# Kernel tuning notes

Measured on AMD Instinct MI355X. Metric: run time of the kernel, lower is better.

The kernel has to match this reference:

```python
import jax, jax.numpy as jnp
import numpy as np

B, T, TR, D, H = 8, 1024, 256, 1024, 16
HS = D // H  # head size = 64
FF = 4 * D


def _ln(x, g, b, eps=1e-5):
    m = jnp.mean(x, axis=-1, keepdims=True)
    v = jnp.mean((x - m) ** 2, axis=-1, keepdims=True)
    return (x - m) * jax.lax.rsqrt(v + eps) * g + b


def setup_inputs() -> dict:
    key = jax.random.key(0)
    ks = jax.random.split(key, 24)
    w = lambda i, shape: jax.random.normal(ks[i], shape, dtype=jnp.float32) * 0.02
    return {
        "x": jax.random.normal(ks[0], (B, T, D), dtype=jnp.float32),
        # reduced positional embedding table (gathered by arange == table itself)
        "pos_emb": w(1, (TR, D)),
        # inner standard Block params
        "blk_ln1_g": jnp.ones((D,), jnp.float32), "blk_ln1_b": jnp.zeros((D,), jnp.float32),
        "blk_wq": w(2, (H, D, HS)), "blk_wk": w(3, (H, D, HS)), "blk_wv": w(4, (H, D, HS)),
        "blk_wo": w(5, (D, D)), "blk_bo": jnp.zeros((D,), jnp.float32),
        "blk_ln2_g": jnp.ones((D,), jnp.float32), "blk_ln2_b": jnp.zeros((D,), jnp.float32),
        "blk_w1": w(6, (D, FF)), "blk_b1": jnp.zeros((FF,), jnp.float32),
        "blk_w2": w(7, (FF, D)), "blk_b2": jnp.zeros((D,), jnp.float32),
        # compressing cross-attention params
        "ln1_g": jnp.ones((D,), jnp.float32), "ln1_b": jnp.zeros((D,), jnp.float32),
        "ca_wq": w(8, (H, D, HS)), "ca_wk": w(9, (H, D, HS)), "ca_wv": w(10, (H, D, HS)),
        "ca_wo": w(11, (D, D)), "ca_bo": jnp.zeros((D,), jnp.float32),
        "ln2_g": jnp.ones((D,), jnp.float32), "ln2_b": jnp.zeros((D,), jnp.float32),
        "ff_w1": w(12, (D, FF)), "ff_b1": jnp.zeros((FF,), jnp.float32),
        "ff_w2": w(13, (FF, D)), "ff_b2": jnp.zeros((D,), jnp.float32),
    }


def reference(x, pos_emb, blk_ln1_g, blk_ln1_b, blk_wq, blk_wk, blk_wv, blk_wo, blk_bo,
              blk_ln2_g, blk_ln2_b, blk_w1, blk_b1, blk_w2, blk_b2,
              ln1_g, ln1_b, ca_wq, ca_wk, ca_wv, ca_wo, ca_bo,
              ln2_g, ln2_b, ff_w1, ff_b1, ff_w2, ff_b2):
    b, t, c = x.shape
    scale = c ** -0.5  # matches q @ k^T * c**-0.5 in source

    # ---- inner standard Block: y = x + sa(ln1(x)); y = y + ffwd(ln2(y)) ----
    h = _ln(x, blk_ln1_g, blk_ln1_b)
    q = jnp.einsum('btc,hcs->bhts', h, blk_wq)
    k = jnp.einsum('btc,hcs->bhts', h, blk_wk)
    v = jnp.einsum('btc,hcs->bhts', h, blk_wv)
    wei = jnp.einsum('bhts,bhus->bhtu', q, k) * scale
    causal = jnp.tril(jnp.ones((t, t), dtype=bool))
    wei = jax.nn.softmax(jnp.where(causal, wei, -jnp.inf), axis=-1)
    att = jnp.einsum('bhtu,bhus->bhts', wei, v)
    att = att.transpose(0, 2, 1, 3).reshape(b, t, c) @ blk_wo + blk_bo
    y = x + att
    h2 = _ln(y, blk_ln2_g, blk_ln2_b)
    y = y + (jax.nn.relu(h2 @ blk_w1 + blk_b1) @ blk_w2 + blk_b2)

    # outer residual in CompressingBlock.forward
    x = x + y

    # ---- compressing cross-attention: queries/values from x, keys from pos emb ----
    h1 = _ln(x, ln1_g, ln1_b)
    q = jnp.einsum('btc,hcs->bhts', h1, ca_wq)
    kk = jnp.einsum('rc,hcs->hrs', pos_emb, ca_wk)  # same for every batch
    v = jnp.einsum('btc,hcs->bhts', h1, ca_wv)
    wei = jnp.einsum('bhts,hrs->bhtr', q, kk) * scale  # [b,h,t,tr]
    tr = pos_emb.shape[0]
    mask = jnp.tril(jnp.ones((t, tr), dtype=bool))  # tril[:t,:tr]
    wei = jax.nn.softmax(jnp.where(mask, wei, -jnp.inf), axis=-1)
    # transpose then wei^T @ v -> compressed sequence length tr
    out = jnp.einsum('bhtr,bhts->bhrs', wei, v)
    out = out.transpose(0, 2, 1, 3).reshape(b, tr, c) @ ca_wo + ca_bo

    # ---- final FFN with residual ----
    h3 = _ln(out, ln2_g, ln2_b)
    out = out + (jax.nn.relu(h3 @ ff_w1 + ff_b1) @ ff_w2 + ff_b2)
    return out
```

## Files before the change

kernel.cpp:

```cpp
#include <hip/hip_runtime.h>
#include <stdint.h>

typedef unsigned short u16;
typedef __attribute__((ext_vector_type(8))) short short8;
typedef __attribute__((ext_vector_type(4))) float f32x4;

#define MFMA16(A,B,C) __builtin_amdgcn_mfma_f32_16x16x32_bf16(A,B,C,0,0,0)

static __device__ __forceinline__ u16 f2bf(float f) {
  union { float f; unsigned u; } v; v.f = f;
  unsigned r = v.u + 0x7FFFu + ((v.u >> 16) & 1u);
  return (u16)(r >> 16);
}

static __device__ __forceinline__ void gload16(const void* g, void* l) {
  __builtin_amdgcn_global_load_lds(
      (const __attribute__((address_space(1))) void*)(uintptr_t)g,
      (__attribute__((address_space(3))) void*)(uint32_t)(uintptr_t)l,
      16, 0, 0);
}

static __device__ __forceinline__ int xcd_swz() {
  const int gx = gridDim.x, gy = gridDim.y, nwg = gx * gy;
  const int orig = blockIdx.y * gx + blockIdx.x;
  const int q = nwg >> 3, rm = nwg & 7, xcd = orig & 7, idx = orig >> 3;
  return (xcd < rm ? xcd * (q + 1) : rm * (q + 1) + (xcd - rm) * q) + idx;
}

#define GPH(CUR, STAGE_STMT, TAIL_STMT) do { \
  short8 af_[4], bf_[4]; \
  _Pragma("unroll") \
  for (int mf = 0; mf < 4; ++mf) { \
    const int r = wm0 + mf * 16 + colL; \
    af_[mf] = *(const short8*)&lds[(CUR) + r * 32 + ((kgr ^ ((r >> 1) & 3)) << 3)]; \
  } \
  _Pragma("unroll") \
  for (int nf = 0; nf < 4; ++nf) { \
    const int r = wn0 + nf * 16 + colL; \
    bf_[nf] = *(const short8*)&lds[(CUR) + 4096 + r * 32 + ((kgr ^ ((r >> 1) & 3)) << 3)]; \
  } \
  STAGE_STMT; \
  _Pragma("unroll") \
  for (int mf = 0; mf < 4; ++mf) \
    _Pragma("unroll") \
    for (int nf = 0; nf < 4; ++nf) \
      acc[mf][nf] = MFMA16(af_[mf], bf_[nf], acc[mf][nf]); \
  TAIL_STMT; \
  __builtin_amdgcn_sched_barrier(0); \
  __builtin_amdgcn_s_barrier(); \
  asm volatile("" ::: "memory"); \
} while (0)

__global__ __launch_bounds__(256) void gemm128p(
    const u16* __restrict__ A, const u16* __restrict__ Wt,
    float* __restrict__ Cf, u16* __restrict__ Cb,
    const float* __restrict__ bias,
    const float* __restrict__ res1, const float* __restrict__ res2,
    int M, int N, int K, int relu)
{
  __shared__ u16 lds[24576];
  const int tid = threadIdx.x;
  const int wid = tid >> 6, lane = tid & 63;
  const int colL = lane & 15, kgr = lane >> 4;
  const int wm0 = (wid & 1) * 64, wn0 = (wid >> 1) * 64;
  const int w = xcd_swz();
  const int m0 = (w / gridDim.y) * 128, n0 = (w % gridDim.y) * 128;
  const int U = K >> 5;
  f32x4 acc[4][4] = {};

  auto stageP = [&](int u, int bufo) {
    const int kb = u * 32;
#pragma unroll
    for (int i = 0; i < 2; ++i) {
      const int c = i * 256 + tid;
      const int row = c >> 2, slot = c & 3;
      const int cs = kb + ((slot ^ ((row >> 1) & 3)) << 3);
      gload16(A  + (size_t)(m0 + row) * K + cs,
              &lds[bufo + ((i * 256 + wid * 64) << 3)]);
      gload16(Wt + (size_t)(n0 + row) * K + cs,
              &lds[bufo + 4096 + ((i * 256 + wid * 64) << 3)]);
    }
  };

  int c0 = 0, c1 = 8192, c2 = 16384;
  stageP(0, c0); stageP(1, c1);
  asm volatile("s_waitcnt vmcnt(4)" ::: "memory");
  __builtin_amdgcn_s_barrier();
  asm volatile("" ::: "memory");

  for (int u = 0; u < U; ++u) {
    GPH(c0,
        { if (u + 2 < U) stageP(u + 2, c2); },
        { if (u + 2 < U) { asm volatile("s_waitcnt vmcnt(4)" ::: "memory"); }
          else           { asm volatile("s_waitcnt vmcnt(0)" ::: "memory"); } });
    const int tmp = c0; c0 = c1; c1 = c2; c2 = tmp;
  }

#pragma unroll
  for (int mf = 0; mf < 4; ++mf) {
#pragma unroll
    for (int nf = 0; nf < 4; ++nf) {
      const int n = n0 + wn0 + nf * 16 + colL;
      const float bv = bias ? bias[n] : 0.f;
#pragma unroll
      for (int rr = 0; rr < 4; ++rr) {
        const int m = m0 + wm0 + mf * 16 + kgr * 4 + rr;
        const size_t off = (size_t)m * N + n;
        float v = acc[mf][nf][rr] + bv;
        if (res1) v += res1[off];
        if (res2) v += res2[off];
        if (relu) v = fmaxf(v, 0.f);
        if (Cf) Cf[off] = v; else Cb[off] = f2bf(v);
      }
    }
  }
}

__global__ __launch_bounds__(256) void ln_rows(
    const float* __restrict__ x, const float* __restrict__ g,
    const float* __restrict__ bt, u16* __restrict__ out)
{
  const int row = blockIdx.x, tid = threadIdx.x;
  const float4 v = ((const float4*)(x + (size_t)row * 1024))[tid];
  float s  = v.x + v.y + v.z + v.w;
  float ss = v.x * v.x + v.y * v.y + v.z * v.z + v.w * v.w;
#pragma unroll
  for (int off = 32; off; off >>= 1) {
    s  += __shfl_xor(s, off);
    ss += __shfl_xor(ss, off);
  }
  __shared__ float red[8];
  const int wid = tid >> 6, lane = tid & 63;
  if (lane == 0) { red[wid] = s; red[4 + wid] = ss; }
  __syncthreads();
  s  = red[0] + red[1] + red[2] + red[3];
  ss = red[4] + red[5] + red[6] + red[7];
  const float mean = s * 0.0009765625f;
  const float var  = ss * 0.0009765625f - mean * mean;
  const float rstd = rsqrtf(var + 1e-5f);
  const float4 gg = ((const float4*)g)[tid];
  const float4 bb = ((const float4*)bt)[tid];
  uint2 ov;
  ov.x = (unsigned)f2bf((v.x - mean) * rstd * gg.x + bb.x) |
         ((unsigned)f2bf((v.y - mean) * rstd * gg.y + bb.y) << 16);
  ov.y = (unsigned)f2bf((v.z - mean) * rstd * gg.z + bb.z) |
         ((unsigned)f2bf((v.w - mean) * rstd * gg.w + bb.w) << 16);
  *(uint2*)(out + (size_t)row * 1024 + tid * 4) = ov;
}

__global__ __launch_bounds__(256) void transpose_w(
    const float* __restrict__ in, u16* __restrict__ out, int R, int C)
{
  __shared__ float t[32][33];
  const int c0 = blockIdx.x * 32, r0 = blockIdx.y * 32;
  const int tx = threadIdx.x & 31, ty = threadIdx.x >> 5;
#pragma unroll
  for (int i = 0; i < 32; i += 8)
    t[ty + i][tx] = in[(size_t)(r0 + ty + i) * C + c0 + tx];
  __syncthreads();
#pragma unroll
  for (int i = 0; i < 32; i += 8)
    out[(size_t)(c0 + ty + i) * R + r0 + tx] = f2bf(t[tx][ty + i]);
}

__global__ __launch_bounds__(256) void pack_head_w(
    const float* __restrict__ w, u16* __restrict__ out)
{
  __shared__ float t[32][33];
  const int h = blockIdx.z;
  const int s0 = blockIdx.x * 32, c0 = blockIdx.y * 32;
  const int tx = threadIdx.x & 31, ty = threadIdx.x >> 5;
#pragma unroll
  for (int i = 0; i < 32; i += 8)
    t[ty + i][tx] = w[((size_t)h * 1024 + c0 + ty + i) * 64 + s0 + tx];
  __syncthreads();
#pragma unroll
  for (int i = 0; i < 32; i += 8)
    out[((size_t)h * 64 + s0 + ty + i) * 1024 + c0 + tx] = f2bf(t[tx][ty + i]);
}

__global__ __launch_bounds__(256) void cvt_bf16(
    const float* __restrict__ in, u16* __restrict__ out)
{
  const int i = blockIdx.x * blockDim.x + threadIdx.x;
  const float4 v = ((const float4*)in)[i];
  uint2 ov;
  ov.x = (unsigned)f2bf(v.x) | ((unsigned)f2bf(v.y) << 16);
  ov.y = (unsigned)f2bf(v.z) | ((unsigned)f2bf(v.w) << 16);
  *(uint2*)(out + (size_t)i * 4) = ov;
}

__global__ __launch_bounds__(256) void vtrans(
    const u16* __restrict__ src, u16* __restrict__ dst, int coloff, int ld)
{
  __shared__ u16 tile[64][65];
  const int t0 = blockIdx.x * 64, h = blockIdx.y, b = blockIdx.z;
  const int lr = threadIdx.x >> 4;
  const int lc = (threadIdx.x & 15) * 4;
#pragma unroll
  for (int i = 0; i < 64; i += 16) {
    const u16* sp = src + (size_t)(b * 1024 + t0 + lr + i) * ld + coloff + h * 64 + lc;
    const uint2 v = *(const uint2*)sp;
    tile[lr + i][lc + 0] = (u16)(v.x & 0xffff);
    tile[lr + i][lc + 1] = (u16)(v.x >> 16);
    tile[lr + i][lc + 2] = (u16)(v.y & 0xffff);
    tile[lr + i][lc + 3] = (u16)(v.y >> 16);
  }
  __syncthreads();
#pragma unroll
  for (int i = 0; i < 64; i += 16) {
    const int s = lr + i;
    uint2 ov;
    ov.x = (unsigned)tile[lc + 0][s] | ((unsigned)tile[lc + 1][s] << 16);
    ov.y = (unsigned)tile[lc + 2][s] | ((unsigned)tile[lc + 3][s] << 16);
    *(uint2*)(dst + (size_t)((b * 16 + h) * 64 + s) * 1024 + t0 + lc) = ov;
  }
}

__global__ __launch_bounds__(512) void attn_inner(
    const u16* __restrict__ qkv, const u16* __restrict__ vt,
    u16* __restrict__ att)
{
  __shared__ u16 Kl[128 * 64];
  __shared__ u16 Vl[64 * 128];
  __shared__ u16 Pl[8 * 16 * 128];
  const int p = blockIdx.x, h = blockIdx.y, b = blockIdx.z;
  const int tid = threadIdx.x, wid = tid >> 6, lane = tid & 63;
  const int col = lane & 15, kgr = lane >> 4;
  const float scale = 0.03125f;
  u16* pw = &Pl[wid * 2048];

  auto run_q = [&](int tb) {
    short8 qf[2];
    {
      const int trow = tb * 128 + wid * 16 + col;
      const u16* qp = qkv + (size_t)(b * 1024 + trow) * 3072 + h * 64 + kgr * 8;
      qf[0] = *(const short8*)qp;
      qf[1] = *(const short8*)(qp + 32);
    }
    f32x4 o[4] = {};
    float mrun[4], lrun[4];
#pragma unroll
    for (int r = 0; r < 4; ++r) { mrun[r] = -1e30f; lrun[r] = 0.f; }

    for (int kt = 0; kt <= tb * 128; kt += 128) {
#pragma unroll
      for (int i = 0; i < 2; ++i) {
        const int e = i * 4096 + tid * 8;
        const int rk = e >> 6, uk = (e >> 3) & 7;
        gload16(qkv + (size_t)(b * 1024 + kt + rk) * 3072 + 1024 + h * 64 +
                    ((uk ^ (rk & 7)) << 3),
                &Kl[i * 4096 + wid * 512]);
        const int rv = e >> 7, uv = (e >> 3) & 15;
        gload16(vt + (size_t)((b * 16 + h) * 64 + rv) * 1024 + kt +
                    ((uv ^ (rv & 7)) << 3),
                &Vl[i * 4096 + wid * 512]);
      }
      __syncthreads();
      f32x4 s[8];
      __builtin_amdgcn_s_setprio(1);
#pragma unroll
      for (int nt = 0; nt < 8; ++nt) {
        const int rk = nt * 16 + col;
        const short8 k0 = *(const short8*)&Kl[rk * 64 + ((kgr ^ (rk & 7)) << 3)];
        const short8 k1 = *(const short8*)&Kl[rk * 64 + (((kgr + 4) ^ (rk & 7)) << 3)];
        f32x4 a = {};
        a = MFMA16(qf[0], k0, a);
        a = MFMA16(qf[1], k1, a);
        s[nt] = a;
      }
      __builtin_amdgcn_s_setprio(0);
      float mx[4];
#pragma unroll
      for (int r = 0; r < 4; ++r) mx[r] = -1e30f;
      const int tbase = tb * 128 + wid * 16 + kgr * 4;
      if (kt == tb * 128) {
#pragma unroll
        for (int nt = 0; nt < 8; ++nt) {
          const int kp = kt + nt * 16 + col;
#pragma unroll
          for (int r = 0; r < 4; ++r) {
            float v = s[nt][r] * scale;
            if (kp > tbase + r) v = -1e30f;
            s[nt][r] = v;
            mx[r] = fmaxf(mx[r], v);
          }
        }
      } else {
#pragma unroll
        for (int nt = 0; nt < 8; ++nt)
#pragma unroll
          for (int r = 0; r < 4; ++r) {
            const float v = s[nt][r] * scale;
            s[nt][r] = v;
            mx[r] = fmaxf(mx[r], v);
          }
      }
#pragma unroll
      for (int r = 0; r < 4; ++r)
#pragma unroll
        for (int off = 1; off < 16; off <<= 1)
          mx[r] = fmaxf(mx[r], __shfl_xor(mx[r], off));
      float f[4], rs[4];
#pragma unroll
      for (int r = 0; r < 4; ++r) {
        const float mn = fmaxf(mrun[r], mx[r]);
        f[r] = __expf(mrun[r] - mn);
        mrun[r] = mn;
        rs[r] = 0.f;
      }
#pragma unroll
      for (int nt = 0; nt < 8; ++nt)
#pragma unroll
        for (int r = 0; r < 4; ++r) {
          const float pv = __expf(s[nt][r] - mrun[r]);
          s[nt][r] = pv;
          rs[r] += pv;
        }
#pragma unroll
      for (int r = 0; r < 4; ++r) {
#pragma unroll
        for (int off = 1; off < 16; off <<= 1)
          rs[r] += __shfl_xor(rs[r], off);
        lrun[r] = lrun[r] * f[r] + rs[r];
      }
#pragma unroll
      for (int st = 0; st < 4; ++st)
#pragma unroll
        for (int r = 0; r < 4; ++r)
          o[st][r] *= f[r];
#pragma unroll
      for (int nt = 0; nt < 8; ++nt)
#pragma unroll
        for (int r = 0; r < 4; ++r) {
          const int rp = kgr * 4 + r;
          pw[rp * 128 + ((nt * 16 + col) ^ ((rp & 7) << 3))] = f2bf(s[nt][r]);
        }
      __builtin_amdgcn_s_setprio(1);
#pragma unroll
      for (int ks = 0; ks < 4; ++ks) {
        const short8 pa = *(const short8*)&pw[col * 128 +
            ((ks * 32 + kgr * 8) ^ ((col & 7) << 3))];
#pragma unroll
        for (int st = 0; st < 4; ++st) {
          const int rv = st * 16 + col;
          const short8 vb = *(const short8*)&Vl[rv * 128 +
              (((ks * 4 + kgr) ^ (rv & 7)) << 3)];
          o[st] = MFMA16(pa, vb, o[st]);
        }
      }
      __builtin_amdgcn_s_setprio(0);
      __syncthreads();
    }
#pragma unroll
    for (int r = 0; r < 4; ++r) {
      const float inv = 1.f / lrun[r];
      const int t = tb * 128 + wid * 16 + kgr * 4 + r;
#pragma unroll
      for (int st = 0; st < 4; ++st)
        att[(size_t)(b * 1024 + t) * 1024 + h * 64 + st * 16 + col] =
            f2bf(o[st][r] * inv);
    }
  };

  run_q(7 - p);
  run_q(p);
}

__global__ __launch_bounds__(512) void attn_cross(
    const u16* __restrict__ qv, const u16* __restrict__ kk,
    const u16* __restrict__ vt, u16* __restrict__ outc)
{
  __shared__ u16 KKl[256 * 64];
  __shared__ u16 Vl[64 * 128];
  __shared__ u16 PTl[256 * 128];
  const int h = blockIdx.x, b = blockIdx.y;
  const int tid = threadIdx.x, wid = tid >> 6, lane = tid & 63;
  const int col = lane & 15, kgr = lane >> 4;
  const float scale = 0.03125f;
#pragma unroll
  for (int i = 0; i < 4; ++i) {
    const int e = i * 4096 + tid * 8;
    const int rk = e >> 6, uk = (e >> 3) & 7;
    gload16(kk + (size_t)rk * 1024 + h * 64 + ((uk ^ (rk & 7)) << 3),
            &KKl[i * 4096 + wid * 512]);
  }
  f32x4 oacc[2][4] = {};
  for (int tt = 0; tt < 8; ++tt) {
    const int t0 = tt * 128;
#pragma unroll
    for (int i = 0; i < 2; ++i) {
      const int e = i * 4096 + tid * 8;
      const int rv = e >> 7, uv = (e >> 3) & 15;
      gload16(vt + (size_t)((b * 16 + h) * 64 + rv) * 1024 + t0 +
                  ((uv ^ (rv & 7)) << 3),
              &Vl[i * 4096 + wid * 512]);
    }
    short8 qf0, qf1;
    {
      const int trow = t0 + wid * 16 + col;
      const u16* qp = qv + (size_t)(b * 1024 + trow) * 2048 + h * 64 + kgr * 8;
      qf0 = *(const short8*)qp;
      qf1 = *(const short8*)(qp + 32);
    }
    __syncthreads();
    f32x4 s[16];
#pragma unroll
    for (int rt = 0; rt < 16; ++rt) {
      const int rk = rt * 16 + col;
      const short8 k0 = *(const short8*)&KKl[rk * 64 + ((kgr ^ (rk & 7)) << 3)];
      const short8 k1 = *(const short8*)&KKl[rk * 64 + (((kgr + 4) ^ (rk & 7)) << 3)];
      f32x4 a = {};
      a = MFMA16(qf0, k0, a);
      a = MFMA16(qf1, k1, a);
      s[rt] = a;
    }
    float mx[4];
#pragma unroll
    for (int r = 0; r < 4; ++r) mx[r] = -1e30f;
    const int tbase = t0 + wid * 16 + kgr * 4;
    if (t0 < 256) {
#pragma unroll
      for (int rt = 0; rt < 16; ++rt) {
        const int rp = rt * 16 + col;
#pragma unroll
        for (int r = 0; r < 4; ++r) {
          float v = s[rt][r] * scale;
          if (rp > tbase + r) v = -1e30f;
          s[rt][r] = v;
          mx[r] = fmaxf(mx[r], v);
        }
      }
    } else {
#pragma unroll
      for (int rt = 0; rt < 16; ++rt)
#pragma unroll
        for (int r = 0; r < 4; ++r) {
          const float v = s[rt][r] * scale;
          s[rt][r] = v;
          mx[r] = fmaxf(mx[r], v);
        }
    }
#pragma unroll
    for (int r = 0; r < 4; ++r)
#pragma unroll
      for (int off = 1; off < 16; off <<= 1)
        mx[r] = fmaxf(mx[r], __shfl_xor(mx[r], off));
    float sm[4];
#pragma unroll
    for (int r = 0; r < 4; ++r) sm[r] = 0.f;
#pragma unroll
    for (int rt = 0; rt < 16; ++rt)
#pragma unroll
      for (int r = 0; r < 4; ++r) {
        const float pv = __expf(s[rt][r] - mx[r]);
        s[rt][r] = pv;
        sm[r] += pv;
      }
#pragma unroll
    for (int r = 0; r < 4; ++r) {
#pragma unroll
      for (int off = 1; off < 16; off <<= 1)
        sm[r] += __shfl_xor(sm[r], off);
      sm[r] = 1.f / sm[r];
    }
#pragma unroll
    for (int rt = 0; rt < 16; ++rt)
#pragma unroll
      for (int r = 0; r < 4; ++r) {
        const int rpt = rt * 16 + col;
        PTl[rpt * 128 + ((wid * 16 + kgr * 4 + r) ^ ((rpt & 7) << 3))] =
            f2bf(s[rt][r] * sm[r]);
      }
    __syncthreads();
#pragma unroll
    for (int rr = 0; rr < 2; ++rr) {
      const int rb = (wid * 2 + rr) * 16;
#pragma unroll
      for (int ks = 0; ks < 4; ++ks) {
        const int rpt = rb + col;
        const short8 pa = *(const short8*)&PTl[rpt * 128 +
            ((ks * 32 + kgr * 8) ^ ((rpt & 7) << 3))];
#pragma unroll
        for (int st = 0; st < 4; ++st) {
          const int rv = st * 16 + col;
          const short8 vb = *(const short8*)&Vl[rv * 128 +
              (((ks * 4 + kgr) ^ (rv & 7)) << 3)];
          oacc[rr][st] = MFMA16(pa, vb, oacc[rr][st]);
        }
      }
    }
    __syncthreads();
  }
#pragma unroll
  for (int rr = 0; rr < 2; ++rr)
#pragma unroll
    for (int st = 0; st < 4; ++st)
#pragma unroll
      for (int r = 0; r < 4; ++r) {
        const int rpos = (wid * 2 + rr) * 16 + kgr * 4 + r;
        outc[(size_t)(b * 256 + rpos) * 1024 + h * 64 + st * 16 + col] =
            f2bf(oacc[rr][st][r]);
      }
}

extern "C" void kernel_launch(void* const* d_in, const int* in_sizes, int n_in,
                              void* d_out, int out_size, void* d_ws, size_t ws_size,
                              hipStream_t stream)
{
  const float* x     = (const float*)d_in[0];
  const float* pos   = (const float*)d_in[1];
  const float* bln1g = (const float*)d_in[2];
  const float* bln1b = (const float*)d_in[3];
  const float* bwq   = (const float*)d_in[4];
  const float* bwk   = (const float*)d_in[5];
  const float* bwv   = (const float*)d_in[6];
  const float* bwo   = (const float*)d_in[7];
  const float* bbo   = (const float*)d_in[8];
  const float* bln2g = (const float*)d_in[9];
  const float* bln2b = (const float*)d_in[10];
  const float* bw1   = (const float*)d_in[11];
  const float* bb1   = (const float*)d_in[12];
  const float* bw2   = (const float*)d_in[13];
  const float* bb2   = (const float*)d_in[14];
  const float* ln1g  = (const float*)d_in[15];
  const float* ln1b  = (const float*)d_in[16];
  const float* cwq   = (const float*)d_in[17];
  const float* cwk   = (const float*)d_in[18];
  const float* cwv   = (const float*)d_in[19];
  const float* cwo   = (const float*)d_in[20];
  const float* cbo   = (const float*)d_in[21];
  const float* cln2g = (const float*)d_in[22];
  const float* cln2b = (const float*)d_in[23];
  const float* fw1   = (const float*)d_in[24];
  const float* fb1   = (const float*)d_in[25];
  const float* fw2   = (const float*)d_in[26];
  const float* fb2   = (const float*)d_in[27];

  char* ws = (char*)d_ws;
  size_t off = 0;
  auto alloc = [&](size_t bytes) -> void* {
    void* p = ws + off; off += (bytes + 255) & ~(size_t)255; return p;
  };
  u16* wqkv_t = (u16*)alloc((size_t)3072 * 1024 * 2);
  u16* wo_t   = (u16*)alloc((size_t)1024 * 1024 * 2);
  u16* w1_t   = (u16*)alloc((size_t)4096 * 1024 * 2);
  u16* w2_t   = (u16*)alloc((size_t)1024 * 4096 * 2);
  u16* cwqv_t = (u16*)alloc((size_t)2048 * 1024 * 2);
  u16* cwk_t  = (u16*)alloc((size_t)1024 * 1024 * 2);
  u16* cwo_t  = (u16*)alloc((size_t)1024 * 1024 * 2);
  u16* fw1_t  = (u16*)alloc((size_t)4096 * 1024 * 2);
  u16* fw2_t  = (u16*)alloc((size_t)1024 * 4096 * 2);
  u16* pos_bf = (u16*)alloc((size_t)256 * 1024 * 2);
  u16* kkb    = (u16*)alloc((size_t)256 * 1024 * 2);
  u16* act_ln = (u16*)alloc((size_t)8192 * 1024 * 2);
  u16* qkv    = (u16*)alloc((size_t)8192 * 3072 * 2);
  u16* att    = (u16*)alloc((size_t)8192 * 1024 * 2);
  u16* ffb    = (u16*)alloc((size_t)8192 * 4096 * 2);
  float* yb   = (float*)alloc((size_t)8192 * 1024 * 4);
  if (ws_size < off) return;
  float* x2   = (float*)qkv;
  u16*   qv   = qkv;
  u16*   vt   = ffb;
  u16*   outc = att;
  float* zb   = yb;
  float* outp = (float*)d_out;

  const dim3 B256(256), B512(512);
  pack_head_w<<<dim3(2, 32, 16), B256, 0, stream>>>(bwq, wqkv_t);
  pack_head_w<<<dim3(2, 32, 16), B256, 0, stream>>>(bwk, wqkv_t + 1024 * 1024);
  pack_head_w<<<dim3(2, 32, 16), B256, 0, stream>>>(bwv, wqkv_t + 2048 * 1024);
  transpose_w<<<dim3(32, 32),  B256, 0, stream>>>(bwo, wo_t, 1024, 1024);
  transpose_w<<<dim3(128, 32), B256, 0, stream>>>(bw1, w1_t, 1024, 4096);
  transpose_w<<<dim3(32, 128), B256, 0, stream>>>(bw2, w2_t, 4096, 1024);
  pack_head_w<<<dim3(2, 32, 16), B256, 0, stream>>>(cwq, cwqv_t);
  pack_head_w<<<dim3(2, 32, 16), B256, 0, stream>>>(cwv, cwqv_t + 1024 * 1024);
  pack_head_w<<<dim3(2, 32, 16), B256, 0, stream>>>(cwk, cwk_t);
  transpose_w<<<dim3(32, 32),  B256, 0, stream>>>(cwo, cwo_t, 1024, 1024);
  transpose_w<<<dim3(128, 32), B256, 0, stream>>>(fw1, fw1_t, 1024, 4096);
  transpose_w<<<dim3(32, 128), B256, 0, stream>>>(fw2, fw2_t, 4096, 1024);
  cvt_bf16<<<dim3(256), B256, 0, stream>>>(pos, pos_bf);

  ln_rows<<<dim3(8192), B256, 0, stream>>>(x, bln1g, bln1b, act_ln);
  gemm128p<<<dim3(64, 24), B256, 0, stream>>>(act_ln, wqkv_t, nullptr, qkv,
      nullptr, nullptr, nullptr, 8192, 3072, 1024, 0);
  vtrans<<<dim3(16, 16, 8), B256, 0, stream>>>(qkv, vt, 2048, 3072);
  attn_inner<<<dim3(4, 16, 8), B512, 0, stream>>>(qkv, vt, att);
  gemm128p<<<dim3(64, 8), B256, 0, stream>>>(att, wo_t, yb, nullptr,
      bbo, x, nullptr, 8192, 1024, 1024, 0);
  ln_rows<<<dim3(8192), B256, 0, stream>>>(yb, bln2g, bln2b, act_ln);
  gemm128p<<<dim3(64, 32), B256, 0, stream>>>(act_ln, w1_t, nullptr, ffb,
      bb1, nullptr, nullptr, 8192, 4096, 1024, 1);
  gemm128p<<<dim3(64, 8), B256, 0, stream>>>(ffb, w2_t, x2, nullptr,
      bb2, yb, x, 8192, 1024, 4096, 0);

  ln_rows<<<dim3(8192), B256, 0, stream>>>(x2, ln1g, ln1b, act_ln);
  gemm128p<<<dim3(64, 16), B256, 0, stream>>>(act_ln, cwqv_t, nullptr, qv,
      nullptr, nullptr, nullptr, 8192, 2048, 1024, 0);
  gemm128p<<<dim3(2, 8), B256, 0, stream>>>(pos_bf, cwk_t, nullptr, kkb,
      nullptr, nullptr, nullptr, 256, 1024, 1024, 0);
  vtrans<<<dim3(16, 16, 8), B256, 0, stream>>>(qv, vt, 1024, 2048);
  attn_cross<<<dim3(16, 8), B512, 0, stream>>>(qv, kkb, vt, outc);
  gemm128p<<<dim3(16, 8), B256, 0, stream>>>(outc, cwo_t, zb, nullptr,
      cbo, nullptr, nullptr, 2048, 1024, 1024, 0);

  ln_rows<<<dim3(2048), B256, 0, stream>>>(zb, cln2g, cln2b, act_ln);
  gemm128p<<<dim3(16, 32), B256, 0, stream>>>(act_ln, fw1_t, nullptr, ffb,
      fb1, nullptr, nullptr, 2048, 4096, 1024, 1);
  gemm128p<<<dim3(16, 8), B256, 0, stream>>>(ffb, fw2_t, outp, nullptr,
      fb2, zb, nullptr, 2048, 1024, 4096, 0);
}
```

Measured before the change: 694.2 us.

## Split cross-attention over query chunks with separate partial-sum reduction kernel

The cross-attention kernel now splits the 1024 query positions into four chunks along a new grid dimension, raising the block count from 128 to 512 to fill more compute units. Each chunk writes fp32 partial outputs into a reused workspace buffer. A new reduce kernel sums the four partials and converts the result to bf16. This trades extra global memory traffic and one more launch for better occupancy of the attention stage.

```diff
diff --git a/kernel.cpp b/kernel.cpp
--- a/kernel.cpp
+++ b/kernel.cpp
@@ -369,12 +369,12 @@
 
 __global__ __launch_bounds__(512) void attn_cross(
     const u16* __restrict__ qv, const u16* __restrict__ kk,
-    const u16* __restrict__ vt, u16* __restrict__ outc)
+    const u16* __restrict__ vt, float* __restrict__ pout)
 {
   __shared__ u16 KKl[256 * 64];
   __shared__ u16 Vl[64 * 128];
   __shared__ u16 PTl[256 * 128];
-  const int h = blockIdx.x, b = blockIdx.y;
+  const int h = blockIdx.x, b = blockIdx.y, ck = blockIdx.z;
   const int tid = threadIdx.x, wid = tid >> 6, lane = tid & 63;
   const int col = lane & 15, kgr = lane >> 4;
   const float scale = 0.03125f;
@@ -386,7 +386,7 @@
             &KKl[i * 4096 + wid * 512]);
   }
   f32x4 oacc[2][4] = {};
-  for (int tt = 0; tt < 8; ++tt) {
+  for (int tt = ck * 2; tt < ck * 2 + 2; ++tt) {
     const int t0 = tt * 128;
 #pragma unroll
     for (int i = 0; i < 2; ++i) {
@@ -499,9 +499,28 @@
 #pragma unroll
       for (int r = 0; r < 4; ++r) {
         const int rpos = (wid * 2 + rr) * 16 + kgr * 4 + r;
-        outc[(size_t)(b * 256 + rpos) * 1024 + h * 64 + st * 16 + col] =
-            f2bf(oacc[rr][st][r]);
-      }
+        pout[(size_t)((ck * 8 + b) * 256 + rpos) * 1024 + h * 64 + st * 16 + col] =
+            oacc[rr][st][r];
+      }
+}
+
+__global__ __launch_bounds__(256) void cross_reduce(
+    const float* __restrict__ pout, u16* __restrict__ outc)
+{
+  const size_t i = ((size_t)blockIdx.x * 256 + threadIdx.x) * 4;
+  const size_t STRIDE = (size_t)8 * 256 * 1024;
+  float4 a = *(const float4*)(pout + i);
+  const float4 b = *(const float4*)(pout + STRIDE + i);
+  const float4 c = *(const float4*)(pout + 2 * STRIDE + i);
+  const float4 d = *(const float4*)(pout + 3 * STRIDE + i);
+  a.x += b.x + c.x + d.x;
+  a.y += b.y + c.y + d.y;
+  a.z += b.z + c.z + d.z;
+  a.w += b.w + c.w + d.w;
+  uint2 ov;
+  ov.x = (unsigned)f2bf(a.x) | ((unsigned)f2bf(a.y) << 16);
+  ov.y = (unsigned)f2bf(a.z) | ((unsigned)f2bf(a.w) << 16);
+  *(uint2*)(outc + i) = ov;
 }
 
 extern "C" void kernel_launch(void* const* d_in, const int* in_sizes, int n_in,
@@ -564,6 +583,7 @@
   u16*   vt   = ffb;
   u16*   outc = att;
   float* zb   = yb;
+  float* pacc = yb;
   float* outp = (float*)d_out;
 
   const dim3 B256(256), B512(512);
@@ -600,7 +620,8 @@
   gemm128p<<<dim3(2, 8), B256, 0, stream>>>(pos_bf, cwk_t, nullptr, kkb,
       nullptr, nullptr, nullptr, 256, 1024, 1024, 0);
   vtrans<<<dim3(16, 16, 8), B256, 0, stream>>>(qv, vt, 1024, 2048);
-  attn_cross<<<dim3(16, 8), B512, 0, stream>>>(qv, kkb, vt, outc);
+  attn_cross<<<dim3(16, 8, 4), B512, 0, stream>>>(qv, kkb, vt, pacc);
+  cross_reduce<<<dim3(2048), B256, 0, stream>>>(pacc, outc);
   gemm128p<<<dim3(16, 8), B256, 0, stream>>>(outc, cwo_t, zb, nullptr,
       cbo, nullptr, nullptr, 2048, 1024, 1024, 0);
 
```

After: 689.4 us. No clear change (-0.7%).
